# Performance work log

Measured on AMD Instinct MI355X. Metric: run time of the kernel, lower is better.

The kernel has to match this reference:

```python
import jax, jax.numpy as jnp
import numpy as np

D = 1024
H = 16
HD = D // H
FF = 4 * D
EPS = 1e-5


def _layernorm(x, g, s):
    m = x.mean(-1, keepdims=True)
    v = ((x - m) ** 2).mean(-1, keepdims=True)  # unbiased=False
    return g * (x - m) / jnp.sqrt(v + EPS) + s


def _gelu_tanh(x):
    c = jnp.sqrt(2.0 / jnp.pi).astype(x.dtype)
    return 0.5 * x * (1 + jnp.tanh(c * (x + 0.044715 * x ** 3)))


def setup_inputs() -> dict:
    key = jax.random.key(0)
    ks = jax.random.split(key, 12)
    B, T = 2, 2048
    std = 0.02
    x = jax.random.normal(ks[0], (B, T, D), jnp.float32)
    wq = jax.random.normal(ks[1], (D, D), jnp.float32) * std
    wk = jax.random.normal(ks[2], (D, D), jnp.float32) * std
    wv = jax.random.normal(ks[3], (D, D), jnp.float32) * std
    wo = jax.random.normal(ks[4], (D, D), jnp.float32) * std
    bo = jnp.zeros((D,), jnp.float32)
    w1 = jax.random.normal(ks[5], (FF, D), jnp.float32) * std
    b1 = jnp.zeros((FF,), jnp.float32)
    w2 = jax.random.normal(ks[6], (D, FF), jnp.float32) * std
    b2 = jnp.zeros((D,), jnp.float32)
    g1 = jnp.ones((D,), jnp.float32)
    s1 = jnp.zeros((D,), jnp.float32)
    g2 = jnp.ones((D,), jnp.float32)
    s2 = jnp.zeros((D,), jnp.float32)
    return {"x": x, "wq": wq, "wk": wk, "wv": wv, "wo": wo, "bo": bo,
            "w1": w1, "b1": b1, "w2": w2, "b2": b2,
            "g1": g1, "s1": s1, "g2": g2, "s2": s2}


def reference(x, wq, wk, wv, wo, bo, w1, b1, w2, b2, g1, s1, g2, s2):
    B, T, _ = x.shape
    # pre-LN attention
    h = _layernorm(x, g1, s1)
    q = (h @ wq.T).reshape(B, T, H, HD).transpose(0, 2, 1, 3)  # [B,H,T,HD]
    k = (h @ wk.T).reshape(B, T, H, HD).transpose(0, 2, 1, 3)
    v = (h @ wv.T).reshape(B, T, H, HD).transpose(0, 2, 1, 3)
    scores = jnp.einsum('bhqd,bhkd->bhqk', q, k)
    causal = jnp.triu(jnp.ones((T, T), bool), k=1)
    scores = jnp.where(causal, -jnp.inf, scores)
    attn = jax.nn.softmax(scores / jnp.sqrt(jnp.float32(HD)), axis=-1)
    ctx = jnp.einsum('bhqk,bhkd->bhqd', attn, v)
    ctx = ctx.transpose(0, 2, 1, 3).reshape(B, T, D)
    x = x + (ctx @ wo.T + bo)
    # pre-LN MLP
    h2 = _layernorm(x, g2, s2)
    ff = _gelu_tanh(h2 @ w1.T + b1) @ w2.T + b2
    return x + ff
```

## Files before the change

### kernel.cpp

```cpp
#include <hip/hip_runtime.h>
#include <hip/hip_bf16.h>
#include <stdint.h>


typedef __attribute__((ext_vector_type(8))) __bf16 bf16x8;
typedef __attribute__((ext_vector_type(4))) __bf16 bf16x4;
typedef __attribute__((ext_vector_type(4))) float  f32x4;

#define DD    1024
#define TSEQ  2048
#define NTOK  4096
#define FFD   4096

#define ASM_VMCNT0() asm volatile("s_waitcnt vmcnt(0)" ::: "memory")

__device__ __forceinline__ void gll16(const void* g, void* l) {
  __builtin_amdgcn_global_load_lds(
      (const __attribute__((address_space(1))) unsigned int*)g,
      (__attribute__((address_space(3))) unsigned int*)l, 16, 0, 0);
}

__device__ __forceinline__ float gelu_f(float v) {
  float u = 0.7978845608028654f * (v + 0.044715f * v * v * v);
  float t = 1.0f - 2.0f / (1.0f + __expf(2.0f * u));
  return 0.5f * v * (1.0f + t);
}

__global__ __launch_bounds__(256) void cvt_weights(
    const float* __restrict__ wq, const float* __restrict__ wk,
    const float* __restrict__ wv, const float* __restrict__ wo,
    const float* __restrict__ w1, const float* __restrict__ w2,
    __bf16* __restrict__ dst)
{
  size_t i4 = (size_t)blockIdx.x * 256 + threadIdx.x;
  size_t e = i4 * 4;
  const float* src; size_t off;
  if (e < (size_t)4 * 1048576) {
    int sel = (int)(e >> 20);
    src = sel == 0 ? wq : sel == 1 ? wk : sel == 2 ? wv : wo;
    off = e & 1048575;
  } else if (e < (size_t)8 * 1048576) {
    src = w1; off = e - (size_t)4 * 1048576;
  } else {
    src = w2; off = e - (size_t)8 * 1048576;
  }
  float4 v = *(const float4*)(src + off);
  bf16x4 o;
  o[0] = (__bf16)v.x; o[1] = (__bf16)v.y; o[2] = (__bf16)v.z; o[3] = (__bf16)v.w;
  *(bf16x4*)(dst + e) = o;
}

__global__ __launch_bounds__(256) void ln_kernel(
    const float* __restrict__ x, const float* __restrict__ gw,
    const float* __restrict__ sw, __bf16* __restrict__ out)
{
  const int row  = blockIdx.x * 4 + (threadIdx.x >> 6);
  const int lane = threadIdx.x & 63;
  const float4* xr = (const float4*)(x + (size_t)row * DD);
  float4 v[4];
  float s = 0.f, sq = 0.f;
#pragma unroll
  for (int i = 0; i < 4; ++i) {
    v[i] = xr[i * 64 + lane];
    s  += v[i].x + v[i].y + v[i].z + v[i].w;
    sq += v[i].x * v[i].x + v[i].y * v[i].y + v[i].z * v[i].z + v[i].w * v[i].w;
  }
#pragma unroll
  for (int off = 32; off >= 1; off >>= 1) {
    s  += __shfl_xor(s, off);
    sq += __shfl_xor(sq, off);
  }
  const float mean = s * (1.f / DD);
  const float rstd = rsqrtf(sq * (1.f / DD) - mean * mean + 1e-5f);
  const float4* gr = (const float4*)gw;
  const float4* sr = (const float4*)sw;
#pragma unroll
  for (int i = 0; i < 4; ++i) {
    float4 gv = gr[i * 64 + lane];
    float4 sv = sr[i * 64 + lane];
    bf16x4 o;
    o[0] = (__bf16)(gv.x * (v[i].x - mean) * rstd + sv.x);
    o[1] = (__bf16)(gv.y * (v[i].y - mean) * rstd + sv.y);
    o[2] = (__bf16)(gv.z * (v[i].z - mean) * rstd + sv.z);
    o[3] = (__bf16)(gv.w * (v[i].w - mean) * rstd + sv.w);
    *(bf16x4*)&out[(size_t)row * DD + (size_t)(i * 64 + lane) * 4] = o;
  }
}

template<int MODE>
__global__ __launch_bounds__(512, 2)
void gemm256(const __bf16* __restrict__ A, int lda,
             const __bf16* __restrict__ Bw, int ldb,
             __bf16* __restrict__ Cout, const float* __restrict__ bias,
             __bf16* __restrict__ voutT, int M, int N, int K)
{
  __shared__ __bf16 sm[65536];
  const int t = threadIdx.x;
  const int lane = t & 63;
  const int l15 = lane & 15, g = lane >> 4;
  const int w = t >> 6;
  const int wm = w >> 2, wn = w & 3;
  const int m0 = blockIdx.y * 256, n0 = blockIdx.x * 256;

  if (MODE == 2) {
    const int kz = blockIdx.z;
    A    += (size_t)kz * 1024;
    Bw   += (size_t)kz * 1024;
    Cout += (size_t)kz * (size_t)M * N;
  }

  const int srow = t >> 3;
  const int schunk = t & 7;
  const int gc = schunk ^ (srow & 7);
  const __bf16* gA = A  + (size_t)(m0 + srow) * lda + gc * 8;
  const __bf16* gB = Bw + (size_t)(n0 + srow) * ldb + gc * 8;
  char* smb = (char*)sm;
  const int sdst = t * 16;

  auto STAGE = [&](int kt, int cur) {
    char* dA = smb + cur * 65536;
    char* dB = dA + 32768;
    const __bf16* a = gA + kt * 64;
    const __bf16* b = gB + kt * 64;
#pragma unroll
    for (int i = 0; i < 4; ++i)
      gll16(a + (size_t)i * 64 * lda, dA + i * 8192 + sdst);
#pragma unroll
    for (int i = 0; i < 4; ++i)
      gll16(b + (size_t)i * 64 * ldb, dB + i * 8192 + sdst);
  };

  const int xa = l15 & 7;
  const int baseA0 = (wm * 128 + l15) * 128 + ((g ^ xa) << 4);
  const int baseA1 = (wm * 128 + l15) * 128 + (((4 + g) ^ xa) << 4);
  const int baseB0 = 32768 + (wn * 64 + l15) * 128 + ((g ^ xa) << 4);
  const int baseB1 = 32768 + (wn * 64 + l15) * 128 + (((4 + g) ^ xa) << 4);

  f32x4 acc[8][4] = {};
  const int NT = K >> 6;

  STAGE(0, 0);
  __syncthreads();

  for (int kt = 0; kt < NT; ++kt) {
    const int cur = kt & 1;
    if (kt + 1 < NT) STAGE(kt + 1, cur ^ 1);

    const char* bufb = smb + cur * 65536;
    bf16x8 af[8][2], bfr[4][2];
#pragma unroll
    for (int mi = 0; mi < 8; ++mi) {
      af[mi][0] = *(const bf16x8*)(bufb + baseA0 + mi * 2048);
      af[mi][1] = *(const bf16x8*)(bufb + baseA1 + mi * 2048);
    }
#pragma unroll
    for (int ni = 0; ni < 4; ++ni) {
      bfr[ni][0] = *(const bf16x8*)(bufb + baseB0 + ni * 2048);
      bfr[ni][1] = *(const bf16x8*)(bufb + baseB1 + ni * 2048);
    }
#pragma unroll
    for (int ks = 0; ks < 2; ++ks)
#pragma unroll
      for (int mi = 0; mi < 8; ++mi)
#pragma unroll
        for (int ni = 0; ni < 4; ++ni)
          acc[mi][ni] = __builtin_amdgcn_mfma_f32_16x16x32_bf16(
              af[mi][ks], bfr[ni][ks], acc[mi][ni], 0, 0, 0);

    __syncthreads();
  }

#pragma unroll
  for (int mi = 0; mi < 8; ++mi) {
    const int rr0 = m0 + wm * 128 + mi * 16 + 4 * g;
#pragma unroll
    for (int ni = 0; ni < 4; ++ni) {
      const int cc = n0 + wn * 64 + ni * 16 + l15;
      if (MODE == 0 && n0 + wn * 64 >= 2048) {
        const int b  = rr0 >> 11;
        const int t0 = rr0 & 2047;
        const int vc = cc - 2048;
        const int h = vc >> 6, d = vc & 63;
        bf16x4 o;
        o[0] = (__bf16)acc[mi][ni][0]; o[1] = (__bf16)acc[mi][ni][1];
        o[2] = (__bf16)acc[mi][ni][2]; o[3] = (__bf16)acc[mi][ni][3];
        *(bf16x4*)&voutT[(((size_t)(b * 16 + h)) * 64 + d) * 2048 + t0] = o;
      } else {
        const int ldc = (MODE == 0) ? 2048 : N;
#pragma unroll
        for (int r = 0; r < 4; ++r) {
          float v = acc[mi][ni][r];
          if (MODE == 0 && cc < 1024) v *= 0.125f;
          if (MODE == 1) { v += bias[cc]; v = gelu_f(v); }
          Cout[(size_t)(rr0 + r) * ldc + cc] = (__bf16)v;
        }
      }
    }
  }
}

__global__ __launch_bounds__(256) void ff2_reduce(
    const __bf16* __restrict__ part, const float* __restrict__ x2,
    const float* __restrict__ b2, float* __restrict__ out)
{
  const size_t e = ((size_t)blockIdx.x * 256 + threadIdx.x) * 4;
  float4 r = *(const float4*)(x2 + e);
  const float4 b = *(const float4*)(b2 + (e & 1023));
  r.x += b.x; r.y += b.y; r.z += b.z; r.w += b.w;
#pragma unroll
  for (int s = 0; s < 4; ++s) {
    bf16x4 p = *(const bf16x4*)(part + (size_t)s * 4194304 + e);
    r.x += (float)p[0]; r.y += (float)p[1]; r.z += (float)p[2]; r.w += (float)p[3];
  }
  *(float4*)(out + e) = r;
}

template<bool BIAS, bool RES>
__global__ __launch_bounds__(256, 3)
void gemm_bt(const __bf16* __restrict__ A, const __bf16* __restrict__ Bw,
             float* __restrict__ Cout, const float* __restrict__ bias,
             const float* __restrict__ res, int M, int N, int K)
{
  __shared__ __bf16 As[128 * 64];
  __shared__ __bf16 Bs[128 * 64];
  const int t    = threadIdx.x;
  const int lane = t & 63;
  const int l15  = lane & 15;
  const int g    = lane >> 4;
  const int w    = t >> 6;
  const int wr   = w >> 1, wc = w & 1;
  const int m0 = blockIdx.y * 128;
  const int n0 = blockIdx.x * 128;
  const int srow = t >> 3;
  const int scol = (t & 7) * 8;

  f32x4 acc[4][4] = {};
  const __bf16* Ap = A  + (size_t)m0 * K;
  const __bf16* Bp = Bw + (size_t)n0 * K;

  for (int k0 = 0; k0 < K; k0 += 64) {
#pragma unroll
    for (int i = 0; i < 4; ++i) {
      const int row = i * 32 + srow;
      gll16(Ap + (size_t)row * K + k0 + scol, &As[row * 64 + scol]);
    }
#pragma unroll
    for (int i = 0; i < 4; ++i) {
      const int row = i * 32 + srow;
      gll16(Bp + (size_t)row * K + k0 + scol, &Bs[row * 64 + scol]);
    }
    __syncthreads();
#pragma unroll
    for (int ks = 0; ks < 2; ++ks) {
      bf16x8 af[4], bfr[4];
#pragma unroll
      for (int mi = 0; mi < 4; ++mi)
        af[mi] = *(const bf16x8*)&As[(wr * 64 + mi * 16 + l15) * 64 + ks * 32 + g * 8];
#pragma unroll
      for (int ni = 0; ni < 4; ++ni)
        bfr[ni] = *(const bf16x8*)&Bs[(wc * 64 + ni * 16 + l15) * 64 + ks * 32 + g * 8];
#pragma unroll
      for (int mi = 0; mi < 4; ++mi)
#pragma unroll
        for (int ni = 0; ni < 4; ++ni)
          acc[mi][ni] = __builtin_amdgcn_mfma_f32_16x16x32_bf16(af[mi], bfr[ni], acc[mi][ni], 0, 0, 0);
    }
    __syncthreads();
  }

  const int crow0 = m0 + wr * 64;
  const int ccol0 = n0 + wc * 64;
#pragma unroll
  for (int mi = 0; mi < 4; ++mi) {
#pragma unroll
    for (int r = 0; r < 4; ++r) {
      const int rr = crow0 + mi * 16 + 4 * g + r;
#pragma unroll
      for (int ni = 0; ni < 4; ++ni) {
        const int cc = ccol0 + ni * 16 + l15;
        float v = acc[mi][ni][r];
        if (BIAS) v += bias[cc];
        if (RES)  v += res[(size_t)rr * N + cc];
        Cout[(size_t)rr * N + cc] = v;
      }
    }
  }
}

__global__ __launch_bounds__(256, 2)
void attn_kernel(const __bf16* __restrict__ qk, const __bf16* __restrict__ vT,
                 __bf16* __restrict__ ctx)
{
  __shared__ __bf16 Ks[64 * 64];
  __shared__ __bf16 VTs[64 * 64];
  __shared__ __bf16 Ps[4][16 * 64];
  const int t    = threadIdx.x;
  const int lane = t & 63;
  const int l15  = lane & 15;
  const int g    = lane >> 4;
  const int w    = t >> 6;
  const int qt = gridDim.x - 1 - blockIdx.x;
  const int hh = blockIdx.y;
  const int bb = blockIdx.z;
  const int q0 = qt * 64;

  const int qrow = q0 + w * 16 + l15;
  const size_t qkrow = ((size_t)(bb * 2048 + qrow)) * 2048 + hh * 64;
  bf16x8 qf0 = *(const bf16x8*)&qk[qkrow + g * 8];
  bf16x8 qf1 = *(const bf16x8*)&qk[qkrow + 32 + g * 8];

  const int kk = t >> 2;
  const int c0 = (t & 3) * 16;
  const __bf16* kbase = &qk[((size_t)(bb * 2048) + kk) * 2048 + 1024 + hh * 64 + c0];
  const __bf16* vbase = &vT[(((size_t)(bb * 16 + hh)) * 64 + kk) * 2048 + c0];
  const int xw  = (kk & 7) << 4;
  char* kdst = (char*)Ks  + kk * 128;
  char* vdst = (char*)VTs + kk * 128;
  const int cw0 = ((((t & 3) * 2)    ) << 4) ^ xw;
  const int cw1 = ((((t & 3) * 2) + 1) << 4) ^ xw;

  f32x4 acc[4] = {};
  float mrun = -1e30f, lrun = 0.f;

  bf16x8 ka0, ka1, va0, va1, kb0, kb1, vb0, vb1;

  auto LOAD = [&](int kt, bf16x8& k0, bf16x8& k1, bf16x8& v0, bf16x8& v1) {
    const __bf16* kp = kbase + (size_t)kt * 64 * 2048;
    k0 = *(const bf16x8*)(kp);
    k1 = *(const bf16x8*)(kp + 8);
    const __bf16* vp = vbase + kt * 64;
    v0 = *(const bf16x8*)(vp);
    v1 = *(const bf16x8*)(vp + 8);
  };
  auto WRITE = [&](bf16x8& k0, bf16x8& k1, bf16x8& v0, bf16x8& v1) {
    *(bf16x8*)(kdst + cw0) = k0;
    *(bf16x8*)(kdst + cw1) = k1;
    *(bf16x8*)(vdst + cw0) = v0;
    *(bf16x8*)(vdst + cw1) = v1;
  };

  const int xr = (l15 & 7) << 4;
  char* pw = (char*)Ps[w] + l15 * 128;

  auto COMPUTE = [&](int kt) {
    f32x4 s[4];
#pragma unroll
    for (int f = 0; f < 4; ++f) {
      const char* kb = (const char*)Ks + (f * 16 + l15) * 128;
      bf16x8 a0 = *(const bf16x8*)(kb + ((g << 4) ^ xr));
      bf16x8 a1 = *(const bf16x8*)(kb + (((4 + g) << 4) ^ xr));
      f32x4 z = {};
      z = __builtin_amdgcn_mfma_f32_16x16x32_bf16(a0, qf0, z, 0, 0, 0);
      z = __builtin_amdgcn_mfma_f32_16x16x32_bf16(a1, qf1, z, 0, 0, 0);
      s[f] = z;
    }

    float pmax = -1e30f;
    if (kt == qt) {
      const int qg = q0 + w * 16 + l15;
#pragma unroll
      for (int f = 0; f < 4; ++f)
#pragma unroll
        for (int r = 0; r < 4; ++r) {
          const int kg = kt * 64 + f * 16 + g * 4 + r;
          if (kg > qg) s[f][r] = -1e30f;
          pmax = fmaxf(pmax, s[f][r]);
        }
    } else {
#pragma unroll
      for (int f = 0; f < 4; ++f)
#pragma unroll
        for (int r = 0; r < 4; ++r) pmax = fmaxf(pmax, s[f][r]);
    }
    pmax = fmaxf(pmax, __shfl_xor(pmax, 16));
    pmax = fmaxf(pmax, __shfl_xor(pmax, 32));

    if (__any(pmax > mrun)) {
      const float mnew  = fmaxf(mrun, pmax);
      const float alpha = __expf(mrun - mnew);
      float al[4];
#pragma unroll
      for (int r = 0; r < 4; ++r) al[r] = __shfl(alpha, g * 4 + r);
#pragma unroll
      for (int nf = 0; nf < 4; ++nf)
#pragma unroll
        for (int r = 0; r < 4; ++r) acc[nf][r] *= al[r];
      lrun *= alpha;
      mrun = mnew;
    }

    float lsum = 0.f;
#pragma unroll
    for (int f = 0; f < 4; ++f)
#pragma unroll
      for (int r = 0; r < 4; ++r) {
        float p = __expf(s[f][r] - mrun);
        s[f][r] = p;
        lsum += p;
      }
    lsum += __shfl_xor(lsum, 16);
    lsum += __shfl_xor(lsum, 32);
    lrun += lsum;

#pragma unroll
    for (int f = 0; f < 4; ++f) {
      bf16x4 pk;
      pk[0] = (__bf16)s[f][0]; pk[1] = (__bf16)s[f][1];
      pk[2] = (__bf16)s[f][2]; pk[3] = (__bf16)s[f][3];
      *(bf16x4*)(pw + ((((f * 2 + (g >> 1)) << 4) ^ xr) + (g & 1) * 8)) = pk;
    }
    asm volatile("s_waitcnt lgkmcnt(0)" ::: "memory");

#pragma unroll
    for (int ks = 0; ks < 2; ++ks) {
      bf16x8 pa = *(const bf16x8*)(pw + (((ks * 4 + g) << 4) ^ xr));
#pragma unroll
      for (int nf = 0; nf < 4; ++nf) {
        const char* vb = (const char*)VTs + (nf * 16 + l15) * 128;
        bf16x8 vf = *(const bf16x8*)(vb + (((ks * 4 + g) << 4) ^ xr));
        acc[nf] = __builtin_amdgcn_mfma_f32_16x16x32_bf16(pa, vf, acc[nf], 0, 0, 0);
      }
    }
  };

  LOAD(0, ka0, ka1, va0, va1);
  int kt = 0;
  for (;;) {
    ASM_VMCNT0();
    __syncthreads();
    WRITE(ka0, ka1, va0, va1);
    if (kt < qt) LOAD(kt + 1, kb0, kb1, vb0, vb1);
    __syncthreads();
    COMPUTE(kt);
    if (++kt > qt) break;

    ASM_VMCNT0();
    __syncthreads();
    WRITE(kb0, kb1, vb0, vb1);
    if (kt < qt) LOAD(kt + 1, ka0, ka1, va0, va1);
    __syncthreads();
    COMPUTE(kt);
    if (++kt > qt) break;
  }

  float li[4];
#pragma unroll
  for (int r = 0; r < 4; ++r) li[r] = 1.0f / __shfl(lrun, g * 4 + r);
#pragma unroll
  for (int nf = 0; nf < 4; ++nf)
#pragma unroll
    for (int r = 0; r < 4; ++r) {
      const int row = q0 + w * 16 + 4 * g + r;
      ctx[((size_t)(bb * 2048 + row)) * DD + hh * 64 + nf * 16 + l15] =
          (__bf16)(acc[nf][r] * li[r]);
    }
}

extern "C" void kernel_launch(void* const* d_in, const int* in_sizes, int n_in,
                              void* d_out, int out_size, void* d_ws, size_t ws_size,
                              hipStream_t stream)
{
  (void)in_sizes; (void)n_in; (void)out_size; (void)ws_size;
  const float* x  = (const float*)d_in[0];
  const float* wq = (const float*)d_in[1];
  const float* wk = (const float*)d_in[2];
  const float* wv = (const float*)d_in[3];
  const float* wo = (const float*)d_in[4];
  const float* bo = (const float*)d_in[5];
  const float* w1 = (const float*)d_in[6];
  const float* b1 = (const float*)d_in[7];
  const float* w2 = (const float*)d_in[8];
  const float* b2 = (const float*)d_in[9];
  const float* g1 = (const float*)d_in[10];
  const float* s1 = (const float*)d_in[11];
  const float* g2 = (const float*)d_in[12];
  const float* s2 = (const float*)d_in[13];
  float* out = (float*)d_out;

  char* ws = (char*)d_ws;
  __bf16* wbf  = (__bf16*)ws;
  __bf16* hbuf = (__bf16*)(ws + 25165824);
  __bf16* qkb  = (__bf16*)(ws + 33554432);
  __bf16* vbT  = (__bf16*)(ws + 50331648);
  __bf16* ctxb = (__bf16*)(ws + 58720256);
  float*  x2   = (float*)(ws + 67108864);
  __bf16* ffb  = (__bf16*)(ws + 83886080);
  __bf16* part = (__bf16*)(ws + 33554432);

  cvt_weights<<<12288, 256, 0, stream>>>(wq, wk, wv, wo, w1, w2, wbf);
  ln_kernel<<<1024, 256, 0, stream>>>(x, g1, s1, hbuf);

  gemm256<0><<<dim3(12, 16), 512, 0, stream>>>(
      hbuf, 1024, wbf, 1024, qkb, nullptr, vbT, NTOK, 3072, 1024);

  dim3 ga(32, 16, 2);
  attn_kernel<<<ga, 256, 0, stream>>>(qkb, vbT, ctxb);

  gemm_bt<true, true><<<dim3(8, 32), 256, 0, stream>>>(
      ctxb, wbf + 3145728, x2, bo, x, NTOK, DD, DD);
  ln_kernel<<<1024, 256, 0, stream>>>(x2, g2, s2, hbuf);

  gemm256<1><<<dim3(16, 16), 512, 0, stream>>>(
      hbuf, 1024, wbf + 4194304, 1024, ffb, b1, nullptr, NTOK, FFD, 1024);

  gemm256<2><<<dim3(4, 16, 4), 512, 0, stream>>>(
      ffb, 4096, wbf + 8388608, 4096, part, nullptr, nullptr, NTOK, DD, 1024);
  ff2_reduce<<<4096, 256, 0, stream>>>(part, x2, b2, out);
}
```

Baseline: 237.1 us.

## Replace 256x256 double-buffered GEMM with 128x128 single-buffered tiles

Changes the three large GEMMs from 256x256 tiles with 512 threads and LDS double buffering to 128x128 tiles with 256 threads and a single LDS buffer. The grids grow fourfold, which gives more blocks per CU for occupancy and better balance across the 256 CUs. The cost is lower data reuse per tile, more global and LDS traffic, and the loss of overlap between global loads and MFMA work inside each block, since every iteration now loads and then synchronises.

```diff
diff --git a/kernel.cpp b/kernel.cpp
--- a/kernel.cpp
+++ b/kernel.cpp
@@ -88,19 +88,19 @@
 }
 
 template<int MODE>
-__global__ __launch_bounds__(512, 2)
-void gemm256(const __bf16* __restrict__ A, int lda,
+__global__ __launch_bounds__(256, 4)
+void gemm128(const __bf16* __restrict__ A, int lda,
              const __bf16* __restrict__ Bw, int ldb,
              __bf16* __restrict__ Cout, const float* __restrict__ bias,
              __bf16* __restrict__ voutT, int M, int N, int K)
 {
-  __shared__ __bf16 sm[65536];
+  __shared__ __bf16 sm[16384];
   const int t = threadIdx.x;
   const int lane = t & 63;
   const int l15 = lane & 15, g = lane >> 4;
   const int w = t >> 6;
-  const int wm = w >> 2, wn = w & 3;
-  const int m0 = blockIdx.y * 256, n0 = blockIdx.x * 256;
+  const int wr = w >> 1, wc = w & 1;
+  const int m0 = blockIdx.y * 128, n0 = blockIdx.x * 128;
 
   if (MODE == 2) {
     const int kz = blockIdx.z;
@@ -117,51 +117,43 @@
   char* smb = (char*)sm;
   const int sdst = t * 16;
 
-  auto STAGE = [&](int kt, int cur) {
-    char* dA = smb + cur * 65536;
-    char* dB = dA + 32768;
+  const int xa = l15 & 7;
+  const int rA = (wr * 64 + l15) * 128;
+  const int rB = 16384 + (wc * 64 + l15) * 128;
+  const int baseA0 = rA + ((g ^ xa) << 4);
+  const int baseA1 = rA + (((4 + g) ^ xa) << 4);
+  const int baseB0 = rB + ((g ^ xa) << 4);
+  const int baseB1 = rB + (((4 + g) ^ xa) << 4);
+
+  f32x4 acc[4][4] = {};
+  const int NT = K >> 6;
+
+  for (int kt = 0; kt < NT; ++kt) {
     const __bf16* a = gA + kt * 64;
     const __bf16* b = gB + kt * 64;
 #pragma unroll
     for (int i = 0; i < 4; ++i)
-      gll16(a + (size_t)i * 64 * lda, dA + i * 8192 + sdst);
+      gll16(a + (size_t)i * 32 * lda, smb + i * 4096 + sdst);
 #pragma unroll
     for (int i = 0; i < 4; ++i)
-      gll16(b + (size_t)i * 64 * ldb, dB + i * 8192 + sdst);
-  };
-
-  const int xa = l15 & 7;
-  const int baseA0 = (wm * 128 + l15) * 128 + ((g ^ xa) << 4);
-  const int baseA1 = (wm * 128 + l15) * 128 + (((4 + g) ^ xa) << 4);
-  const int baseB0 = 32768 + (wn * 64 + l15) * 128 + ((g ^ xa) << 4);
-  const int baseB1 = 32768 + (wn * 64 + l15) * 128 + (((4 + g) ^ xa) << 4);
-
-  f32x4 acc[8][4] = {};
-  const int NT = K >> 6;
-
-  STAGE(0, 0);
-  __syncthreads();
-
-  for (int kt = 0; kt < NT; ++kt) {
-    const int cur = kt & 1;
-    if (kt + 1 < NT) STAGE(kt + 1, cur ^ 1);
-
-    const char* bufb = smb + cur * 65536;
-    bf16x8 af[8][2], bfr[4][2];
-#pragma unroll
-    for (int mi = 0; mi < 8; ++mi) {
-      af[mi][0] = *(const bf16x8*)(bufb + baseA0 + mi * 2048);
-      af[mi][1] = *(const bf16x8*)(bufb + baseA1 + mi * 2048);
+      gll16(b + (size_t)i * 32 * ldb, smb + 16384 + i * 4096 + sdst);
+    __syncthreads();
+
+    bf16x8 af[4][2], bfr[4][2];
+#pragma unroll
+    for (int mi = 0; mi < 4; ++mi) {
+      af[mi][0] = *(const bf16x8*)(smb + baseA0 + mi * 2048);
+      af[mi][1] = *(const bf16x8*)(smb + baseA1 + mi * 2048);
     }
 #pragma unroll
     for (int ni = 0; ni < 4; ++ni) {
-      bfr[ni][0] = *(const bf16x8*)(bufb + baseB0 + ni * 2048);
-      bfr[ni][1] = *(const bf16x8*)(bufb + baseB1 + ni * 2048);
+      bfr[ni][0] = *(const bf16x8*)(smb + baseB0 + ni * 2048);
+      bfr[ni][1] = *(const bf16x8*)(smb + baseB1 + ni * 2048);
     }
 #pragma unroll
     for (int ks = 0; ks < 2; ++ks)
 #pragma unroll
-      for (int mi = 0; mi < 8; ++mi)
+      for (int mi = 0; mi < 4; ++mi)
 #pragma unroll
         for (int ni = 0; ni < 4; ++ni)
           acc[mi][ni] = __builtin_amdgcn_mfma_f32_16x16x32_bf16(
@@ -171,12 +163,12 @@
   }
 
 #pragma unroll
-  for (int mi = 0; mi < 8; ++mi) {
-    const int rr0 = m0 + wm * 128 + mi * 16 + 4 * g;
+  for (int mi = 0; mi < 4; ++mi) {
+    const int rr0 = m0 + wr * 64 + mi * 16 + 4 * g;
 #pragma unroll
     for (int ni = 0; ni < 4; ++ni) {
-      const int cc = n0 + wn * 64 + ni * 16 + l15;
-      if (MODE == 0 && n0 + wn * 64 >= 2048) {
+      const int cc = n0 + wc * 64 + ni * 16 + l15;
+      if (MODE == 0 && n0 >= 2048) {
         const int b  = rr0 >> 11;
         const int t0 = rr0 & 2047;
         const int vc = cc - 2048;
@@ -490,7 +482,7 @@
   cvt_weights<<<12288, 256, 0, stream>>>(wq, wk, wv, wo, w1, w2, wbf);
   ln_kernel<<<1024, 256, 0, stream>>>(x, g1, s1, hbuf);
 
-  gemm256<0><<<dim3(12, 16), 512, 0, stream>>>(
+  gemm128<0><<<dim3(24, 32), 256, 0, stream>>>(
       hbuf, 1024, wbf, 1024, qkb, nullptr, vbT, NTOK, 3072, 1024);
 
   dim3 ga(32, 16, 2);
@@ -500,10 +492,10 @@
       ctxb, wbf + 3145728, x2, bo, x, NTOK, DD, DD);
   ln_kernel<<<1024, 256, 0, stream>>>(x2, g2, s2, hbuf);
 
-  gemm256<1><<<dim3(16, 16), 512, 0, stream>>>(
+  gemm128<1><<<dim3(32, 32), 256, 0, stream>>>(
       hbuf, 1024, wbf + 4194304, 1024, ffb, b1, nullptr, NTOK, FFD, 1024);
 
-  gemm256<2><<<dim3(4, 16, 4), 512, 0, stream>>>(
+  gemm128<2><<<dim3(8, 32, 4), 256, 0, stream>>>(
       ffb, 4096, wbf + 8388608, 4096, part, nullptr, nullptr, NTOK, DD, 1024);
   ff2_reduce<<<4096, 256, 0, stream>>>(part, x2, b2, out);
 }
```

New measurement: 246.5 us. 4.0% more time.

## Pair causal query tiles per attention block to balance work and share K/V loads

Applied to the files above, without the earlier changes.

Each attention block now processes two query tiles, j and 31-j, so every block performs roughly the same number of causal key tiles. Each K/V tile staged into shared memory is reused by both query tiles, which halves global K/V traffic per query. The grid is halved accordingly. The change doubles accumulator and softmax state registers and gives a separate P scratch per tile, which may pressure occupancy.

```diff
diff --git a/kernel.cpp b/kernel.cpp
--- a/kernel.cpp
+++ b/kernel.cpp
@@ -287,27 +287,117 @@
   }
 }
 
+__device__ __forceinline__ void attn_tile(
+    int kt, int qt, int qg,
+    bf16x8 qf0, bf16x8 qf1,
+    f32x4 (&acc)[4], float& mrun, float& lrun,
+    char* pw, const char* KsB, const char* VTsB,
+    int g, int l15, int xr)
+{
+  f32x4 s[4];
+#pragma unroll
+  for (int f = 0; f < 4; ++f) {
+    const char* kb = KsB + (f * 16 + l15) * 128;
+    bf16x8 a0 = *(const bf16x8*)(kb + ((g << 4) ^ xr));
+    bf16x8 a1 = *(const bf16x8*)(kb + (((4 + g) << 4) ^ xr));
+    f32x4 z = {};
+    z = __builtin_amdgcn_mfma_f32_16x16x32_bf16(a0, qf0, z, 0, 0, 0);
+    z = __builtin_amdgcn_mfma_f32_16x16x32_bf16(a1, qf1, z, 0, 0, 0);
+    s[f] = z;
+  }
+
+  float pmax = -1e30f;
+  if (kt == qt) {
+#pragma unroll
+    for (int f = 0; f < 4; ++f)
+#pragma unroll
+      for (int r = 0; r < 4; ++r) {
+        const int kg = kt * 64 + f * 16 + g * 4 + r;
+        if (kg > qg) s[f][r] = -1e30f;
+        pmax = fmaxf(pmax, s[f][r]);
+      }
+  } else {
+#pragma unroll
+    for (int f = 0; f < 4; ++f)
+#pragma unroll
+      for (int r = 0; r < 4; ++r) pmax = fmaxf(pmax, s[f][r]);
+  }
+  pmax = fmaxf(pmax, __shfl_xor(pmax, 16));
+  pmax = fmaxf(pmax, __shfl_xor(pmax, 32));
+
+  if (__any(pmax > mrun)) {
+    const float mnew  = fmaxf(mrun, pmax);
+    const float alpha = __expf(mrun - mnew);
+    float al[4];
+#pragma unroll
+    for (int r = 0; r < 4; ++r) al[r] = __shfl(alpha, g * 4 + r);
+#pragma unroll
+    for (int nf = 0; nf < 4; ++nf)
+#pragma unroll
+      for (int r = 0; r < 4; ++r) acc[nf][r] *= al[r];
+    lrun *= alpha;
+    mrun = mnew;
+  }
+
+  float lsum = 0.f;
+#pragma unroll
+  for (int f = 0; f < 4; ++f)
+#pragma unroll
+    for (int r = 0; r < 4; ++r) {
+      float p = __expf(s[f][r] - mrun);
+      s[f][r] = p;
+      lsum += p;
+    }
+  lsum += __shfl_xor(lsum, 16);
+  lsum += __shfl_xor(lsum, 32);
+  lrun += lsum;
+
+#pragma unroll
+  for (int f = 0; f < 4; ++f) {
+    bf16x4 pk;
+    pk[0] = (__bf16)s[f][0]; pk[1] = (__bf16)s[f][1];
+    pk[2] = (__bf16)s[f][2]; pk[3] = (__bf16)s[f][3];
+    *(bf16x4*)(pw + ((((f * 2 + (g >> 1)) << 4) ^ xr) + (g & 1) * 8)) = pk;
+  }
+  asm volatile("s_waitcnt lgkmcnt(0)" ::: "memory");
+
+#pragma unroll
+  for (int ks = 0; ks < 2; ++ks) {
+    bf16x8 pa = *(const bf16x8*)(pw + (((ks * 4 + g) << 4) ^ xr));
+#pragma unroll
+    for (int nf = 0; nf < 4; ++nf) {
+      const char* vb = VTsB + (nf * 16 + l15) * 128;
+      bf16x8 vf = *(const bf16x8*)(vb + (((ks * 4 + g) << 4) ^ xr));
+      acc[nf] = __builtin_amdgcn_mfma_f32_16x16x32_bf16(pa, vf, acc[nf], 0, 0, 0);
+    }
+  }
+}
+
 __global__ __launch_bounds__(256, 2)
 void attn_kernel(const __bf16* __restrict__ qk, const __bf16* __restrict__ vT,
                  __bf16* __restrict__ ctx)
 {
   __shared__ __bf16 Ks[64 * 64];
   __shared__ __bf16 VTs[64 * 64];
-  __shared__ __bf16 Ps[4][16 * 64];
+  __shared__ __bf16 Ps[4][2][1024];
   const int t    = threadIdx.x;
   const int lane = t & 63;
   const int l15  = lane & 15;
   const int g    = lane >> 4;
   const int w    = t >> 6;
-  const int qt = gridDim.x - 1 - blockIdx.x;
+  const int j  = blockIdx.x;
+  const int qtA = j, qtB = 31 - j;
   const int hh = blockIdx.y;
   const int bb = blockIdx.z;
-  const int q0 = qt * 64;
-
-  const int qrow = q0 + w * 16 + l15;
-  const size_t qkrow = ((size_t)(bb * 2048 + qrow)) * 2048 + hh * 64;
-  bf16x8 qf0 = *(const bf16x8*)&qk[qkrow + g * 8];
-  bf16x8 qf1 = *(const bf16x8*)&qk[qkrow + 32 + g * 8];
+
+  const int qrowA = qtA * 64 + w * 16 + l15;
+  const int qrowB = qtB * 64 + w * 16 + l15;
+  const size_t qkrA = ((size_t)(bb * 2048 + qrowA)) * 2048 + hh * 64;
+  const size_t qkrB = ((size_t)(bb * 2048 + qrowB)) * 2048 + hh * 64;
+  bf16x8 qfA0 = *(const bf16x8*)&qk[qkrA + g * 8];
+  bf16x8 qfA1 = *(const bf16x8*)&qk[qkrA + 32 + g * 8];
+  bf16x8 qfB0 = *(const bf16x8*)&qk[qkrB + g * 8];
+  bf16x8 qfB1 = *(const bf16x8*)&qk[qkrB + 32 + g * 8];
 
   const int kk = t >> 2;
   const int c0 = (t & 3) * 16;
@@ -319,8 +409,10 @@
   const int cw0 = ((((t & 3) * 2)    ) << 4) ^ xw;
   const int cw1 = ((((t & 3) * 2) + 1) << 4) ^ xw;
 
-  f32x4 acc[4] = {};
-  float mrun = -1e30f, lrun = 0.f;
+  f32x4 accA[4] = {}, accB[4] = {};
+  float mA = -1e30f, lA = 0.f, mB = -1e30f, lB = 0.f;
+  const int qgA = qtA * 64 + w * 16 + l15;
+  const int qgB = qtB * 64 + w * 16 + l15;
 
   bf16x8 ka0, ka1, va0, va1, kb0, kb1, vb0, vb1;
 
@@ -340,119 +432,52 @@
   };
 
   const int xr = (l15 & 7) << 4;
-  char* pw = (char*)Ps[w] + l15 * 128;
-
-  auto COMPUTE = [&](int kt) {
-    f32x4 s[4];
-#pragma unroll
-    for (int f = 0; f < 4; ++f) {
-      const char* kb = (const char*)Ks + (f * 16 + l15) * 128;
-      bf16x8 a0 = *(const bf16x8*)(kb + ((g << 4) ^ xr));
-      bf16x8 a1 = *(const bf16x8*)(kb + (((4 + g) << 4) ^ xr));
-      f32x4 z = {};
-      z = __builtin_amdgcn_mfma_f32_16x16x32_bf16(a0, qf0, z, 0, 0, 0);
-      z = __builtin_amdgcn_mfma_f32_16x16x32_bf16(a1, qf1, z, 0, 0, 0);
-      s[f] = z;
-    }
-
-    float pmax = -1e30f;
-    if (kt == qt) {
-      const int qg = q0 + w * 16 + l15;
-#pragma unroll
-      for (int f = 0; f < 4; ++f)
-#pragma unroll
-        for (int r = 0; r < 4; ++r) {
-          const int kg = kt * 64 + f * 16 + g * 4 + r;
-          if (kg > qg) s[f][r] = -1e30f;
-          pmax = fmaxf(pmax, s[f][r]);
-        }
-    } else {
-#pragma unroll
-      for (int f = 0; f < 4; ++f)
-#pragma unroll
-        for (int r = 0; r < 4; ++r) pmax = fmaxf(pmax, s[f][r]);
-    }
-    pmax = fmaxf(pmax, __shfl_xor(pmax, 16));
-    pmax = fmaxf(pmax, __shfl_xor(pmax, 32));
-
-    if (__any(pmax > mrun)) {
-      const float mnew  = fmaxf(mrun, pmax);
-      const float alpha = __expf(mrun - mnew);
-      float al[4];
-#pragma unroll
-      for (int r = 0; r < 4; ++r) al[r] = __shfl(alpha, g * 4 + r);
-#pragma unroll
-      for (int nf = 0; nf < 4; ++nf)
-#pragma unroll
-        for (int r = 0; r < 4; ++r) acc[nf][r] *= al[r];
-      lrun *= alpha;
-      mrun = mnew;
-    }
-
-    float lsum = 0.f;
-#pragma unroll
-    for (int f = 0; f < 4; ++f)
-#pragma unroll
-      for (int r = 0; r < 4; ++r) {
-        float p = __expf(s[f][r] - mrun);
-        s[f][r] = p;
-        lsum += p;
-      }
-    lsum += __shfl_xor(lsum, 16);
-    lsum += __shfl_xor(lsum, 32);
-    lrun += lsum;
-
-#pragma unroll
-    for (int f = 0; f < 4; ++f) {
-      bf16x4 pk;
-      pk[0] = (__bf16)s[f][0]; pk[1] = (__bf16)s[f][1];
-      pk[2] = (__bf16)s[f][2]; pk[3] = (__bf16)s[f][3];
-      *(bf16x4*)(pw + ((((f * 2 + (g >> 1)) << 4) ^ xr) + (g & 1) * 8)) = pk;
-    }
-    asm volatile("s_waitcnt lgkmcnt(0)" ::: "memory");
-
-#pragma unroll
-    for (int ks = 0; ks < 2; ++ks) {
-      bf16x8 pa = *(const bf16x8*)(pw + (((ks * 4 + g) << 4) ^ xr));
-#pragma unroll
-      for (int nf = 0; nf < 4; ++nf) {
-        const char* vb = (const char*)VTs + (nf * 16 + l15) * 128;
-        bf16x8 vf = *(const bf16x8*)(vb + (((ks * 4 + g) << 4) ^ xr));
-        acc[nf] = __builtin_amdgcn_mfma_f32_16x16x32_bf16(pa, vf, acc[nf], 0, 0, 0);
-      }
-    }
-  };
-
+  char* pwA = (char*)&Ps[w][0][0] + l15 * 128;
+  char* pwB = (char*)&Ps[w][1][0] + l15 * 128;
+  const char* KsB  = (const char*)Ks;
+  const char* VTsB = (const char*)VTs;
+
+  const int NT = qtB + 1;
   LOAD(0, ka0, ka1, va0, va1);
   int kt = 0;
   for (;;) {
     ASM_VMCNT0();
     __syncthreads();
     WRITE(ka0, ka1, va0, va1);
-    if (kt < qt) LOAD(kt + 1, kb0, kb1, vb0, vb1);
-    __syncthreads();
-    COMPUTE(kt);
-    if (++kt > qt) break;
+    if (kt + 1 < NT) LOAD(kt + 1, kb0, kb1, vb0, vb1);
+    __syncthreads();
+    attn_tile(kt, qtB, qgB, qfB0, qfB1, accB, mB, lB, pwB, KsB, VTsB, g, l15, xr);
+    if (kt <= qtA)
+      attn_tile(kt, qtA, qgA, qfA0, qfA1, accA, mA, lA, pwA, KsB, VTsB, g, l15, xr);
+    if (++kt >= NT) break;
 
     ASM_VMCNT0();
     __syncthreads();
     WRITE(kb0, kb1, vb0, vb1);
-    if (kt < qt) LOAD(kt + 1, ka0, ka1, va0, va1);
-    __syncthreads();
-    COMPUTE(kt);
-    if (++kt > qt) break;
-  }
-
-  float li[4];
-#pragma unroll
-  for (int r = 0; r < 4; ++r) li[r] = 1.0f / __shfl(lrun, g * 4 + r);
+    if (kt + 1 < NT) LOAD(kt + 1, ka0, ka1, va0, va1);
+    __syncthreads();
+    attn_tile(kt, qtB, qgB, qfB0, qfB1, accB, mB, lB, pwB, KsB, VTsB, g, l15, xr);
+    if (kt <= qtA)
+      attn_tile(kt, qtA, qgA, qfA0, qfA1, accA, mA, lA, pwA, KsB, VTsB, g, l15, xr);
+    if (++kt >= NT) break;
+  }
+
+  float liA[4], liB[4];
+#pragma unroll
+  for (int r = 0; r < 4; ++r) {
+    liA[r] = 1.0f / __shfl(lA, g * 4 + r);
+    liB[r] = 1.0f / __shfl(lB, g * 4 + r);
+  }
 #pragma unroll
   for (int nf = 0; nf < 4; ++nf)
 #pragma unroll
     for (int r = 0; r < 4; ++r) {
-      const int row = q0 + w * 16 + 4 * g + r;
-      ctx[((size_t)(bb * 2048 + row)) * DD + hh * 64 + nf * 16 + l15] =
-          (__bf16)(acc[nf][r] * li[r]);
+      const int rowA = qtA * 64 + w * 16 + 4 * g + r;
+      const int rowB = qtB * 64 + w * 16 + 4 * g + r;
+      ctx[((size_t)(bb * 2048 + rowA)) * DD + hh * 64 + nf * 16 + l15] =
+          (__bf16)(accA[nf][r] * liA[r]);
+      ctx[((size_t)(bb * 2048 + rowB)) * DD + hh * 64 + nf * 16 + l15] =
+          (__bf16)(accB[nf][r] * liB[r]);
     }
 }
 
@@ -493,7 +518,7 @@
   gemm256<0><<<dim3(12, 16), 512, 0, stream>>>(
       hbuf, 1024, wbf, 1024, qkb, nullptr, vbT, NTOK, 3072, 1024);
 
-  dim3 ga(32, 16, 2);
+  dim3 ga(16, 16, 2);
   attn_kernel<<<ga, 256, 0, stream>>>(qkb, vbT, ctxb);
 
   gemm_bt<true, true><<<dim3(8, 32), 256, 0, stream>>>(
```

New measurement: 219.1 us. -7.6%, faster.
